# Kernel optimization log

Hardware: AMD Instinct MI355X
Metric: run time of the kernel (lower is better)

Reference implementation:

```python
import jax, jax.numpy as jnp
import numpy as np

N = 50000          # num_nodes
E = 600000         # num_edges
D_IN = 128         # gcn_embed_dims[0]
D_H = 128          # gcn_embed_dims[1]
D_OUT = 64         # gcn_embed_dims[2]
D_MLP = 64         # mlp hidden


def setup_inputs() -> dict:
    key = jax.random.key(0)
    ks = jax.random.split(key, 10)
    s = lambda fan: 1.0 / np.sqrt(fan).astype(np.float32)
    return {
        "X": jax.random.normal(ks[0], (N, D_IN), jnp.float32),
        "edges": jax.random.randint(ks[1], (2, E), 0, N, dtype=jnp.int32),
        # GCN layer 1
        "Wg1": jax.random.normal(ks[2], (D_IN, D_H), jnp.float32) * s(D_IN),
        "bg1": jnp.zeros((D_H,), jnp.float32),
        # GCN layer 2
        "Wg2": jax.random.normal(ks[3], (D_H, D_OUT), jnp.float32) * s(D_H),
        "bg2": jnp.zeros((D_OUT,), jnp.float32),
        # decoder MLP: in = 2*D_OUT = 128
        "Wm1": jax.random.normal(ks[4], (2 * D_OUT, D_MLP), jnp.float32) * s(2 * D_OUT),
        "bm1": jnp.zeros((D_MLP,), jnp.float32),
        "Wm2": jax.random.normal(ks[5], (D_MLP, 1), jnp.float32) * s(D_MLP),
        "bm2": jnp.zeros((1,), jnp.float32),
    }


def gcn_conv(X, W, b, src, dst):
    """GCNConv: out = D^{-1/2} (A + I) D^{-1/2} X W + b (PyG semantics)."""
    n = X.shape[0]
    XW = X @ W                                   # [N, d_out]
    loop = jnp.arange(n, dtype=src.dtype)
    src2 = jnp.concatenate([src, loop])          # add self-loops
    dst2 = jnp.concatenate([dst, loop])
    deg = jax.ops.segment_sum(jnp.ones_like(dst2, dtype=XW.dtype), dst2,
                              num_segments=n)    # in-degree incl. self-loop
    dinv = jax.lax.rsqrt(jnp.maximum(deg, 1.0))  # deg >= 1 due to self-loop
    norm = dinv[src2] * dinv[dst2]               # [E+N]
    out = jax.ops.segment_sum(XW[src2] * norm[:, None], dst2, num_segments=n)
    return out + b


def reference(X, edges, Wg1, bg1, Wg2, bg2, Wm1, bm1, Wm2, bm2):
    src, dst = edges[0], edges[1]
    # encode: GCNConv -> ReLU -> GCNConv
    H = jax.nn.relu(gcn_conv(X, Wg1, bg1, src, dst))
    H = gcn_conv(H, Wg2, bg2, src, dst)          # [N, 64]
    # decode: gather endpoints, concat, MLP
    Z = jnp.concatenate([H[src], H[dst]], axis=-1)  # [E, 128]
    Z = jax.nn.relu(Z @ Wm1 + bm1)                   # [E, 64]
    return Z @ Wm2 + bm2                             # [E, 1]
```

## Files before the change

### kernel.cpp

```cpp
#include <hip/hip_runtime.h>


typedef __attribute__((ext_vector_type(8))) short s8v;
typedef __attribute__((ext_vector_type(4))) float f4v;

__device__ __forceinline__ ushort f2bf(float x) {
    unsigned u = __float_as_uint(x);
    unsigned r = (u + 0x7fffu + ((u >> 16) & 1u)) >> 16;
    return (ushort)r;
}
__device__ __forceinline__ float bf2f(ushort h) {
    return __uint_as_float(((unsigned)h) << 16);
}

__global__ void count_deg_k(const int* __restrict__ dst, int* __restrict__ cnt, int E) {
    int i = blockIdx.x * 256 + threadIdx.x;
    if (i < E) atomicAdd(&cnt[dst[i]], 1);
}

__global__ void dinv_k(const int* __restrict__ cnt, float* __restrict__ dinv, int n) {
    int i = blockIdx.x * 256 + threadIdx.x;
    if (i < n) dinv[i] = rsqrtf((float)cnt[i] + 1.0f);
}

__global__ void scan1_k(const int* __restrict__ cnt, int* __restrict__ excl,
                        int* __restrict__ bsum, int n) {
    __shared__ int sd[256];
    int t = threadIdx.x;
    int base = blockIdx.x * 1024 + t * 4;
    int v0 = 0, v1 = 0, v2 = 0, v3 = 0;
    if (base + 0 < n) v0 = cnt[base + 0];
    if (base + 1 < n) v1 = cnt[base + 1];
    if (base + 2 < n) v2 = cnt[base + 2];
    if (base + 3 < n) v3 = cnt[base + 3];
    int sum = v0 + v1 + v2 + v3;
    int acc = sum;
    sd[t] = acc;
    __syncthreads();
    for (int off = 1; off < 256; off <<= 1) {
        int x = (t >= off) ? sd[t - off] : 0;
        __syncthreads();
        acc += x;
        sd[t] = acc;
        __syncthreads();
    }
    int run = acc - sum;
    if (base + 0 < n) excl[base + 0] = run;
    run += v0;
    if (base + 1 < n) excl[base + 1] = run;
    run += v1;
    if (base + 2 < n) excl[base + 2] = run;
    run += v2;
    if (base + 3 < n) excl[base + 3] = run;
    if (t == 255) bsum[blockIdx.x] = acc;
}

__global__ void scan2_k(int* __restrict__ bsum, int nb) {
    __shared__ int sd[256];
    int t = threadIdx.x;
    int v = (t < nb) ? bsum[t] : 0;
    int acc = v;
    sd[t] = acc;
    __syncthreads();
    for (int off = 1; off < 256; off <<= 1) {
        int x = (t >= off) ? sd[t - off] : 0;
        __syncthreads();
        acc += x;
        sd[t] = acc;
        __syncthreads();
    }
    if (t < nb) bsum[t] = acc - v;
}

__global__ void scan3_k(int* __restrict__ excl, const int* __restrict__ bsum,
                        int* __restrict__ cursor, int n) {
    int i = blockIdx.x * 256 + threadIdx.x;
    if (i < n) {
        int v = excl[i] + bsum[i >> 10];
        excl[i] = v;
        cursor[i] = v;
    }
}

__global__ void scatter_k(const int* __restrict__ src, const int* __restrict__ dst,
                          int* __restrict__ cursor, int2* __restrict__ csr_se, int E) {
    int i = blockIdx.x * 256 + threadIdx.x;
    if (i < E) {
        int d = dst[i];
        int p = atomicAdd(&cursor[d], 1);
        int2 se; se.x = src[i]; se.y = i;
        csr_se[p] = se;
    }
}

__global__ void split_k(const float* __restrict__ X, ushort* __restrict__ Xh,
                        ushort* __restrict__ Xl, int n4) {
    int i = blockIdx.x * 256 + threadIdx.x;
    if (i >= n4) return;
    float4 v = ((const float4*)X)[i];
    ushort4 h, l;
    h.x = f2bf(v.x); l.x = f2bf(v.x - bf2f(h.x));
    h.y = f2bf(v.y); l.y = f2bf(v.y - bf2f(h.y));
    h.z = f2bf(v.z); l.z = f2bf(v.z - bf2f(h.z));
    h.w = f2bf(v.w); l.w = f2bf(v.w - bf2f(h.w));
    ((ushort4*)Xh)[i] = h;
    ((ushort4*)Xl)[i] = l;
}

__global__ void wtsplit_k(const float* __restrict__ W, ushort* __restrict__ Wth,
                          ushort* __restrict__ Wtl) {
    int i = blockIdx.x * 256 + threadIdx.x;
    int n = i >> 7, k = i & 127;
    float x = W[k * 128 + n];
    ushort h = f2bf(x);
    Wth[i] = h;
    Wtl[i] = f2bf(x - bf2f(h));
}

__global__ void wfold_k(const float* __restrict__ Wg2, const float* __restrict__ bg2,
                        const float* __restrict__ Wm1,
                        ushort* __restrict__ Wfth, ushort* __restrict__ Wftl,
                        float* __restrict__ bcat) {
    int i = blockIdx.x * 256 + threadIdx.x;
    if (i < 128 * 128) {
        int r = i >> 7, c = i & 127;
        const float* wc = (c < 64) ? (Wm1 + c) : (Wm1 + 64 * 64 + (c - 64));
        float acc = 0.f;
#pragma unroll 8
        for (int j = 0; j < 64; ++j) acc = fmaf(Wg2[r * 64 + j], wc[j * 64], acc);
        ushort h = f2bf(acc);
        Wfth[c * 128 + r] = h;
        Wftl[c * 128 + r] = f2bf(acc - bf2f(h));
    } else if (i < 128 * 128 + 128) {
        int c = i - 128 * 128;
        const float* wc = (c < 64) ? (Wm1 + c) : (Wm1 + 64 * 64 + (c - 64));
        float acc = 0.f;
#pragma unroll 8
        for (int j = 0; j < 64; ++j) acc = fmaf(bg2[j], wc[j * 64], acc);
        bcat[c] = acc;
    }
}

__global__ __launch_bounds__(256) void mgemm_k(
    const ushort* __restrict__ Ah, const ushort* __restrict__ Al,
    const ushort* __restrict__ Bth, const ushort* __restrict__ Btl,
    const float* __restrict__ rowscale, float* __restrict__ C, int M) {
    __shared__ ushort Bs[2][128][136];
    const int t = threadIdx.x;
#pragma unroll
    for (int i = 0; i < 16; ++i) {
        int c = i * 256 + t;
        int arr = c >> 11;
        int cc = c & 2047;
        int n = cc >> 4, kb = cc & 15;
        const ushort* src = arr ? Btl : Bth;
        s8v v = *(const s8v*)(src + n * 128 + kb * 8);
        *(s8v*)(&Bs[arr][n][kb * 8]) = v;
    }
    __syncthreads();

    const int lane = t & 63;
    const int w = t >> 6;
    const int r16 = lane & 15;
    const int kg = lane >> 4;
    int arow = blockIdx.x * 64 + w * 16 + r16;
    if (arow >= M) arow = M - 1;
    const ushort* pAh = Ah + (size_t)arow * 128 + kg * 8;
    const ushort* pAl = Al + (size_t)arow * 128 + kg * 8;

    f4v acc[8];
#pragma unroll
    for (int ct = 0; ct < 8; ++ct) acc[ct] = (f4v){0.f, 0.f, 0.f, 0.f};

#pragma unroll
    for (int ks = 0; ks < 4; ++ks) {
        s8v ah = *(const s8v*)(pAh + ks * 32);
        s8v al = *(const s8v*)(pAl + ks * 32);
#pragma unroll
        for (int ct = 0; ct < 8; ++ct) {
            s8v bh = *(const s8v*)(&Bs[0][ct * 16 + r16][ks * 32 + kg * 8]);
            s8v bl = *(const s8v*)(&Bs[1][ct * 16 + r16][ks * 32 + kg * 8]);
            acc[ct] = __builtin_amdgcn_mfma_f32_16x16x32_bf16(ah, bh, acc[ct], 0, 0, 0);
            acc[ct] = __builtin_amdgcn_mfma_f32_16x16x32_bf16(ah, bl, acc[ct], 0, 0, 0);
            acc[ct] = __builtin_amdgcn_mfma_f32_16x16x32_bf16(al, bh, acc[ct], 0, 0, 0);
        }
    }

    const int rbase = blockIdx.x * 64 + w * 16 + kg * 4;
#pragma unroll
    for (int r = 0; r < 4; ++r) {
        int row = rbase + r;
        if (row < M) {
            float sc = rowscale[row];
#pragma unroll
            for (int ct = 0; ct < 8; ++ct)
                C[(size_t)row * 128 + ct * 16 + r16] = acc[ct][r] * sc;
        }
    }
}

template <bool RELU_BF16>
__global__ void agg128_k(const float* __restrict__ XW, const float* __restrict__ dinv,
                         const int* __restrict__ row_start, const int* __restrict__ cnt,
                         const int2* __restrict__ csr_se, const float* __restrict__ bias,
                         float* __restrict__ outf, ushort* __restrict__ outh,
                         ushort* __restrict__ outl, int n) {
    int wid = (int)((blockIdx.x * blockDim.x + threadIdx.x) >> 6);
    int lane = threadIdx.x & 63;
    if (wid >= n) return;
    float di = dinv[wid];
    int deg = cnt[wid];
    int rs = row_start[wid];
    const float2* base = (const float2*)XW;
    float2 a = base[(size_t)wid * 64 + lane];
    float ax = a.x, ay = a.y;
    int i = 0;
    while (i < deg) {
        int take = deg - i;
        if (take > 64) take = 64;
        int addr = rs + i + lane;
        int lim = rs + deg - 1;
        if (addr > lim) addr = lim;
        int vidx = csr_se[addr].x;
        int j = 0;
        for (; j + 8 <= take; j += 8) {
            int s0 = __shfl(vidx, j + 0), s1 = __shfl(vidx, j + 1);
            int s2 = __shfl(vidx, j + 2), s3 = __shfl(vidx, j + 3);
            int s4 = __shfl(vidx, j + 4), s5 = __shfl(vidx, j + 5);
            int s6 = __shfl(vidx, j + 6), s7 = __shfl(vidx, j + 7);
            float2 u0 = base[(size_t)s0 * 64 + lane];
            float2 u1 = base[(size_t)s1 * 64 + lane];
            float2 u2 = base[(size_t)s2 * 64 + lane];
            float2 u3 = base[(size_t)s3 * 64 + lane];
            float2 u4 = base[(size_t)s4 * 64 + lane];
            float2 u5 = base[(size_t)s5 * 64 + lane];
            float2 u6 = base[(size_t)s6 * 64 + lane];
            float2 u7 = base[(size_t)s7 * 64 + lane];
            ax += ((u0.x + u1.x) + (u2.x + u3.x)) + ((u4.x + u5.x) + (u6.x + u7.x));
            ay += ((u0.y + u1.y) + (u2.y + u3.y)) + ((u4.y + u5.y) + (u6.y + u7.y));
        }
        for (; j + 2 <= take; j += 2) {
            int s0 = __shfl(vidx, j + 0), s1 = __shfl(vidx, j + 1);
            float2 u0 = base[(size_t)s0 * 64 + lane];
            float2 u1 = base[(size_t)s1 * 64 + lane];
            ax += u0.x + u1.x;
            ay += u0.y + u1.y;
        }
        if (j < take) {
            int s = __shfl(vidx, j);
            float2 u = base[(size_t)s * 64 + lane];
            ax += u.x;
            ay += u.y;
        }
        i += take;
    }
    float2 b = ((const float2*)bias)[lane];
    ax = fmaf(ax, di, b.x);
    ay = fmaf(ay, di, b.y);
    if constexpr (RELU_BF16) {
        ax = fmaxf(ax, 0.f);
        ay = fmaxf(ay, 0.f);
        ushort2 h, l;
        h.x = f2bf(ax); l.x = f2bf(ax - bf2f(h.x));
        h.y = f2bf(ay); l.y = f2bf(ay - bf2f(h.y));
        ((ushort2*)outh)[(size_t)wid * 64 + lane] = h;
        ((ushort2*)outl)[(size_t)wid * 64 + lane] = l;
    } else {
        float2 r; r.x = ax; r.y = ay;
        ((float2*)outf)[(size_t)wid * 64 + lane] = r;
    }
}

__global__ __launch_bounds__(256) void edge_mlp2_k(
    const float* __restrict__ PQ, const int* __restrict__ row_start,
    const int* __restrict__ cnt, const int2* __restrict__ csr_se,
    const float* __restrict__ bm1, const float* __restrict__ w2,
    const float* __restrict__ bm2, float* __restrict__ out, int n) {
    int wid = (int)((blockIdx.x * blockDim.x + threadIdx.x) >> 6);
    int lane = threadIdx.x & 63;
    if (wid >= n) return;
    int deg = cnt[wid];
    if (deg == 0) return;
    int rs = row_start[wid];
    const int sub = lane >> 4;
    const int q = lane & 15;

    const float4 b1v = ((const float4*)bm1)[q];
    const float4 w2v = ((const float4*)w2)[q];
    const float b2 = bm2[0];
    float4 Qv = *(const float4*)(PQ + (size_t)wid * 128 + 64 + q * 4);
    float4 bq;
    bq.x = Qv.x + b1v.x; bq.y = Qv.y + b1v.y;
    bq.z = Qv.z + b1v.z; bq.w = Qv.w + b1v.w;

    int i = 0;
    while (i < deg) {
        int take = deg - i;
        if (take > 64) take = 64;
        int addr = rs + i + lane;
        int lim = rs + deg - 1;
        if (addr > lim) addr = lim;
        int2 se = csr_se[addr];
        for (int j = 0; j < take; j += 8) {
            int ia = j + sub;
            int ib = j + 4 + sub;
            bool aa = ia < take;
            bool ab = ib < take;
            int sa = __shfl(se.x, aa ? ia : 0);
            int ea = __shfl(se.y, aa ? ia : 0);
            int sb = __shfl(se.x, ab ? ib : 0);
            int eb = __shfl(se.y, ab ? ib : 0);
            float4 pa = *(const float4*)(PQ + (size_t)sa * 128 + q * 4);
            float4 pb = *(const float4*)(PQ + (size_t)sb * 128 + q * 4);
            float ha0 = fmaxf(pa.x + bq.x, 0.f);
            float ha1 = fmaxf(pa.y + bq.y, 0.f);
            float ha2 = fmaxf(pa.z + bq.z, 0.f);
            float ha3 = fmaxf(pa.w + bq.w, 0.f);
            float hb0 = fmaxf(pb.x + bq.x, 0.f);
            float hb1 = fmaxf(pb.y + bq.y, 0.f);
            float hb2 = fmaxf(pb.z + bq.z, 0.f);
            float hb3 = fmaxf(pb.w + bq.w, 0.f);
            float va = fmaf(ha0, w2v.x, fmaf(ha1, w2v.y, fmaf(ha2, w2v.z, ha3 * w2v.w)));
            float vb = fmaf(hb0, w2v.x, fmaf(hb1, w2v.y, fmaf(hb2, w2v.z, hb3 * w2v.w)));
            va += __shfl_xor(va, 8, 16);
            va += __shfl_xor(va, 4, 16);
            va += __shfl_xor(va, 2, 16);
            va += __shfl_xor(va, 1, 16);
            vb += __shfl_xor(vb, 8, 16);
            vb += __shfl_xor(vb, 4, 16);
            vb += __shfl_xor(vb, 2, 16);
            vb += __shfl_xor(vb, 1, 16);
            if (aa && q == 0) out[ea] = va + b2;
            if (ab && q == 0) out[eb] = vb + b2;
        }
        i += take;
    }
}


extern "C" void kernel_launch(void* const* d_in, const int* in_sizes, int n_in,
                              void* d_out, int out_size, void* d_ws, size_t ws_size,
                              hipStream_t stream) {
    const float* X   = (const float*)d_in[0];
    const int*  edges = (const int*)d_in[1];
    const float* Wg1 = (const float*)d_in[2];
    const float* bg1 = (const float*)d_in[3];
    const float* Wg2 = (const float*)d_in[4];
    const float* bg2 = (const float*)d_in[5];
    const float* Wm1 = (const float*)d_in[6];
    const float* bm1 = (const float*)d_in[7];
    const float* Wm2 = (const float*)d_in[8];
    const float* bm2 = (const float*)d_in[9];
    float* out = (float*)d_out;

    const int N = in_sizes[0] / 128;
    const int E = in_sizes[1] / 2;
    const int* esrc = edges;
    const int* edst = edges + E;

    char* p = (char*)d_ws;
    auto alloc = [&](size_t nbytes) {
        void* r = (void*)p;
        p += (nbytes + 255) & ~(size_t)255;
        return r;
    };
    float* bufA   = (float*)alloc((size_t)N * 128 * 4);
    float* bufB   = (float*)alloc((size_t)N * 128 * 4);
    float* dinv   = (float*)alloc((size_t)N * 4);
    int* cnt      = (int*)alloc((size_t)N * 4);
    int* rowst    = (int*)alloc((size_t)N * 4);
    int* cursor   = (int*)alloc((size_t)N * 4);
    int* bsum     = (int*)alloc(1024);
    ushort* Wg1th = (ushort*)alloc(128 * 128 * 2);
    ushort* Wg1tl = (ushort*)alloc(128 * 128 * 2);
    ushort* Wfth  = (ushort*)alloc(128 * 128 * 2);
    ushort* Wftl  = (ushort*)alloc(128 * 128 * 2);
    float* bcat   = (float*)alloc(128 * 4);
    int2* csr_se  = (int2*)alloc((size_t)E * 8);
    (void)ws_size; (void)n_in; (void)out_size;

    const size_t NF = (size_t)N * 128;
    ushort* Xh = (ushort*)bufB;
    ushort* Xl = Xh + NF;
    ushort* Hh = Xh;
    ushort* Hl = Xl;

    const int gE = (E + 255) / 256;
    const int gN = (N + 255) / 256;
    const int nb = (N + 1023) / 1024;
    const int gM64 = (N + 63) / 64;
    const int gAgg = (N * 64 + 255) / 256;
    const int n4 = (int)(NF / 4);
    const int gSplit = (n4 + 255) / 256;

    hipMemsetAsync(cnt, 0, (size_t)N * 4, stream);
    count_deg_k<<<gE, 256, 0, stream>>>(edst, cnt, E);
    dinv_k<<<gN, 256, 0, stream>>>(cnt, dinv, N);
    scan1_k<<<nb, 256, 0, stream>>>(cnt, rowst, bsum, N);
    scan2_k<<<1, 256, 0, stream>>>(bsum, nb);
    scan3_k<<<gN, 256, 0, stream>>>(rowst, bsum, cursor, N);
    scatter_k<<<gE, 256, 0, stream>>>(esrc, edst, cursor, csr_se, E);
    wtsplit_k<<<64, 256, 0, stream>>>(Wg1, Wg1th, Wg1tl);
    wfold_k<<<65, 256, 0, stream>>>(Wg2, bg2, Wm1, Wfth, Wftl, bcat);
    split_k<<<gSplit, 256, 0, stream>>>(X, Xh, Xl, n4);

    mgemm_k<<<gM64, 256, 0, stream>>>(Xh, Xl, Wg1th, Wg1tl, dinv, bufA, N);
    agg128_k<true><<<gAgg, 256, 0, stream>>>(bufA, dinv, rowst, cnt, csr_se, bg1,
                                             nullptr, Hh, Hl, N);
    mgemm_k<<<gM64, 256, 0, stream>>>(Hh, Hl, Wfth, Wftl, dinv, bufA, N);
    agg128_k<false><<<gAgg, 256, 0, stream>>>(bufA, dinv, rowst, cnt, csr_se, bcat,
                                              bufB, nullptr, nullptr, N);
    edge_mlp2_k<<<gAgg, 256, 0, stream>>>(bufB, rowst, cnt, csr_se, bm1, Wm2, bm2, out, N);
}
```

Baseline: 314.0 us.

## Fuse bf16 split into GEMM and store intermediate features as bf16

```diff
diff --git a/kernel.cpp b/kernel.cpp
--- a/kernel.cpp
+++ b/kernel.cpp
@@ -1,30 +1,30 @@
 #include <hip/hip_runtime.h>
 
 
-typedef __attribute__((ext_vector_type(8))) short s8v;
-typedef __attribute__((ext_vector_type(4))) float f4v;
-
-__device__ __forceinline__ ushort f2bf(float x) {
+typedef __attribute__((ext_vector_type(8))) short bf8v;
+typedef __attribute__((ext_vector_type(4))) float fa4v;
+
+__device__ __forceinline__ ushort to_bf(float x) {
     unsigned u = __float_as_uint(x);
     unsigned r = (u + 0x7fffu + ((u >> 16) & 1u)) >> 16;
     return (ushort)r;
 }
-__device__ __forceinline__ float bf2f(ushort h) {
+__device__ __forceinline__ float from_bf(ushort h) {
     return __uint_as_float(((unsigned)h) << 16);
 }
 
-__global__ void count_deg_k(const int* __restrict__ dst, int* __restrict__ cnt, int E) {
+__global__ void deg_count_k(const int* __restrict__ dst, int* __restrict__ cnt, int E) {
     int i = blockIdx.x * 256 + threadIdx.x;
     if (i < E) atomicAdd(&cnt[dst[i]], 1);
 }
 
-__global__ void dinv_k(const int* __restrict__ cnt, float* __restrict__ dinv, int n) {
+__global__ void deg_inv_k(const int* __restrict__ cnt, float* __restrict__ dinv, int n) {
     int i = blockIdx.x * 256 + threadIdx.x;
     if (i < n) dinv[i] = rsqrtf((float)cnt[i] + 1.0f);
 }
 
-__global__ void scan1_k(const int* __restrict__ cnt, int* __restrict__ excl,
-                        int* __restrict__ bsum, int n) {
+__global__ void scan_a_k(const int* __restrict__ cnt, int* __restrict__ excl,
+                         int* __restrict__ bsum, int n) {
     __shared__ int sd[256];
     int t = threadIdx.x;
     int base = blockIdx.x * 1024 + t * 4;
@@ -55,7 +55,7 @@
     if (t == 255) bsum[blockIdx.x] = acc;
 }
 
-__global__ void scan2_k(int* __restrict__ bsum, int nb) {
+__global__ void scan_b_k(int* __restrict__ bsum, int nb) {
     __shared__ int sd[256];
     int t = threadIdx.x;
     int v = (t < nb) ? bsum[t] : 0;
@@ -72,8 +72,8 @@
     if (t < nb) bsum[t] = acc - v;
 }
 
-__global__ void scan3_k(int* __restrict__ excl, const int* __restrict__ bsum,
-                        int* __restrict__ cursor, int n) {
+__global__ void scan_c_k(int* __restrict__ excl, const int* __restrict__ bsum,
+                         int* __restrict__ cursor, int n) {
     int i = blockIdx.x * 256 + threadIdx.x;
     if (i < n) {
         int v = excl[i] + bsum[i >> 10];
@@ -82,8 +82,8 @@
     }
 }
 
-__global__ void scatter_k(const int* __restrict__ src, const int* __restrict__ dst,
-                          int* __restrict__ cursor, int2* __restrict__ csr_se, int E) {
+__global__ void csr_fill_k(const int* __restrict__ src, const int* __restrict__ dst,
+                           int* __restrict__ cursor, int2* __restrict__ csr_se, int E) {
     int i = blockIdx.x * 256 + threadIdx.x;
     if (i < E) {
         int d = dst[i];
@@ -93,34 +93,20 @@
     }
 }
 
-__global__ void split_k(const float* __restrict__ X, ushort* __restrict__ Xh,
-                        ushort* __restrict__ Xl, int n4) {
-    int i = blockIdx.x * 256 + threadIdx.x;
-    if (i >= n4) return;
-    float4 v = ((const float4*)X)[i];
-    ushort4 h, l;
-    h.x = f2bf(v.x); l.x = f2bf(v.x - bf2f(h.x));
-    h.y = f2bf(v.y); l.y = f2bf(v.y - bf2f(h.y));
-    h.z = f2bf(v.z); l.z = f2bf(v.z - bf2f(h.z));
-    h.w = f2bf(v.w); l.w = f2bf(v.w - bf2f(h.w));
-    ((ushort4*)Xh)[i] = h;
-    ((ushort4*)Xl)[i] = l;
-}
-
-__global__ void wtsplit_k(const float* __restrict__ W, ushort* __restrict__ Wth,
-                          ushort* __restrict__ Wtl) {
+__global__ void w1t_split_k(const float* __restrict__ W, ushort* __restrict__ Wth,
+                            ushort* __restrict__ Wtl) {
     int i = blockIdx.x * 256 + threadIdx.x;
     int n = i >> 7, k = i & 127;
     float x = W[k * 128 + n];
-    ushort h = f2bf(x);
+    ushort h = to_bf(x);
     Wth[i] = h;
-    Wtl[i] = f2bf(x - bf2f(h));
-}
-
-__global__ void wfold_k(const float* __restrict__ Wg2, const float* __restrict__ bg2,
-                        const float* __restrict__ Wm1,
-                        ushort* __restrict__ Wfth, ushort* __restrict__ Wftl,
-                        float* __restrict__ bcat) {
+    Wtl[i] = to_bf(x - from_bf(h));
+}
+
+__global__ void wfold_split_k(const float* __restrict__ Wg2, const float* __restrict__ bg2,
+                              const float* __restrict__ Wm1,
+                              ushort* __restrict__ Wfth, ushort* __restrict__ Wftl,
+                              float* __restrict__ bcat) {
     int i = blockIdx.x * 256 + threadIdx.x;
     if (i < 128 * 128) {
         int r = i >> 7, c = i & 127;
@@ -128,9 +114,9 @@
         float acc = 0.f;
 #pragma unroll 8
         for (int j = 0; j < 64; ++j) acc = fmaf(Wg2[r * 64 + j], wc[j * 64], acc);
-        ushort h = f2bf(acc);
+        ushort h = to_bf(acc);
         Wfth[c * 128 + r] = h;
-        Wftl[c * 128 + r] = f2bf(acc - bf2f(h));
+        Wftl[c * 128 + r] = to_bf(acc - from_bf(h));
     } else if (i < 128 * 128 + 128) {
         int c = i - 128 * 128;
         const float* wc = (c < 64) ? (Wm1 + c) : (Wm1 + 64 * 64 + (c - 64));
@@ -141,10 +127,10 @@
     }
 }
 
-__global__ __launch_bounds__(256) void mgemm_k(
-    const ushort* __restrict__ Ah, const ushort* __restrict__ Al,
+__global__ __launch_bounds__(256) void gemm_mfma_k(
+    const float* __restrict__ A,
     const ushort* __restrict__ Bth, const ushort* __restrict__ Btl,
-    const float* __restrict__ rowscale, float* __restrict__ C, int M) {
+    const float* __restrict__ rowscale, ushort* __restrict__ C, int M) {
     __shared__ ushort Bs[2][128][136];
     const int t = threadIdx.x;
 #pragma unroll
@@ -154,8 +140,8 @@
         int cc = c & 2047;
         int n = cc >> 4, kb = cc & 15;
         const ushort* src = arr ? Btl : Bth;
-        s8v v = *(const s8v*)(src + n * 128 + kb * 8);
-        *(s8v*)(&Bs[arr][n][kb * 8]) = v;
+        bf8v v = *(const bf8v*)(src + n * 128 + kb * 8);
+        *(bf8v*)(&Bs[arr][n][kb * 8]) = v;
     }
     __syncthreads();
 
@@ -165,21 +151,28 @@
     const int kg = lane >> 4;
     int arow = blockIdx.x * 64 + w * 16 + r16;
     if (arow >= M) arow = M - 1;
-    const ushort* pAh = Ah + (size_t)arow * 128 + kg * 8;
-    const ushort* pAl = Al + (size_t)arow * 128 + kg * 8;
-
-    f4v acc[8];
-#pragma unroll
-    for (int ct = 0; ct < 8; ++ct) acc[ct] = (f4v){0.f, 0.f, 0.f, 0.f};
+    const float* pA = A + (size_t)arow * 128 + kg * 8;
+
+    fa4v acc[8];
+#pragma unroll
+    for (int ct = 0; ct < 8; ++ct) acc[ct] = (fa4v){0.f, 0.f, 0.f, 0.f};
 
 #pragma unroll
     for (int ks = 0; ks < 4; ++ks) {
-        s8v ah = *(const s8v*)(pAh + ks * 32);
-        s8v al = *(const s8v*)(pAl + ks * 32);
+        float av[8];
+        *(float4*)(&av[0]) = *(const float4*)(pA + ks * 32);
+        *(float4*)(&av[4]) = *(const float4*)(pA + ks * 32 + 4);
+        bf8v ah, al;
+#pragma unroll
+        for (int j = 0; j < 8; ++j) {
+            ushort h = to_bf(av[j]);
+            ah[j] = (short)h;
+            al[j] = (short)to_bf(av[j] - from_bf(h));
+        }
 #pragma unroll
         for (int ct = 0; ct < 8; ++ct) {
-            s8v bh = *(const s8v*)(&Bs[0][ct * 16 + r16][ks * 32 + kg * 8]);
-            s8v bl = *(const s8v*)(&Bs[1][ct * 16 + r16][ks * 32 + kg * 8]);
+            bf8v bh = *(const bf8v*)(&Bs[0][ct * 16 + r16][ks * 32 + kg * 8]);
+            bf8v bl = *(const bf8v*)(&Bs[1][ct * 16 + r16][ks * 32 + kg * 8]);
             acc[ct] = __builtin_amdgcn_mfma_f32_16x16x32_bf16(ah, bh, acc[ct], 0, 0, 0);
             acc[ct] = __builtin_amdgcn_mfma_f32_16x16x32_bf16(ah, bl, acc[ct], 0, 0, 0);
             acc[ct] = __builtin_amdgcn_mfma_f32_16x16x32_bf16(al, bh, acc[ct], 0, 0, 0);
@@ -194,26 +187,24 @@
             float sc = rowscale[row];
 #pragma unroll
             for (int ct = 0; ct < 8; ++ct)
-                C[(size_t)row * 128 + ct * 16 + r16] = acc[ct][r] * sc;
-        }
-    }
-}
-
-template <bool RELU_BF16>
-__global__ void agg128_k(const float* __restrict__ XW, const float* __restrict__ dinv,
-                         const int* __restrict__ row_start, const int* __restrict__ cnt,
-                         const int2* __restrict__ csr_se, const float* __restrict__ bias,
-                         float* __restrict__ outf, ushort* __restrict__ outh,
-                         ushort* __restrict__ outl, int n) {
+                C[(size_t)row * 128 + ct * 16 + r16] = to_bf(acc[ct][r] * sc);
+        }
+    }
+}
+
+template <bool RELU, bool BF16OUT>
+__global__ void gcn_agg_k(const ushort* __restrict__ Cb, const float* __restrict__ dinv,
+                          const int* __restrict__ row_start, const int* __restrict__ cnt,
+                          const int2* __restrict__ csr_se, const float* __restrict__ bias,
+                          float* __restrict__ outf, ushort* __restrict__ outh, int n) {
     int wid = (int)((blockIdx.x * blockDim.x + threadIdx.x) >> 6);
     int lane = threadIdx.x & 63;
     if (wid >= n) return;
     float di = dinv[wid];
     int deg = cnt[wid];
     int rs = row_start[wid];
-    const float2* base = (const float2*)XW;
-    float2 a = base[(size_t)wid * 64 + lane];
-    float ax = a.x, ay = a.y;
+    ushort2 a = *(const ushort2*)(Cb + (size_t)wid * 128 + lane * 2);
+    float ax = from_bf(a.x), ay = from_bf(a.y);
     int i = 0;
     while (i < deg) {
         int take = deg - i;
@@ -228,51 +219,54 @@
             int s2 = __shfl(vidx, j + 2), s3 = __shfl(vidx, j + 3);
             int s4 = __shfl(vidx, j + 4), s5 = __shfl(vidx, j + 5);
             int s6 = __shfl(vidx, j + 6), s7 = __shfl(vidx, j + 7);
-            float2 u0 = base[(size_t)s0 * 64 + lane];
-            float2 u1 = base[(size_t)s1 * 64 + lane];
-            float2 u2 = base[(size_t)s2 * 64 + lane];
-            float2 u3 = base[(size_t)s3 * 64 + lane];
-            float2 u4 = base[(size_t)s4 * 64 + lane];
-            float2 u5 = base[(size_t)s5 * 64 + lane];
-            float2 u6 = base[(size_t)s6 * 64 + lane];
-            float2 u7 = base[(size_t)s7 * 64 + lane];
-            ax += ((u0.x + u1.x) + (u2.x + u3.x)) + ((u4.x + u5.x) + (u6.x + u7.x));
-            ay += ((u0.y + u1.y) + (u2.y + u3.y)) + ((u4.y + u5.y) + (u6.y + u7.y));
+            ushort2 u0 = *(const ushort2*)(Cb + (size_t)s0 * 128 + lane * 2);
+            ushort2 u1 = *(const ushort2*)(Cb + (size_t)s1 * 128 + lane * 2);
+            ushort2 u2 = *(const ushort2*)(Cb + (size_t)s2 * 128 + lane * 2);
+            ushort2 u3 = *(const ushort2*)(Cb + (size_t)s3 * 128 + lane * 2);
+            ushort2 u4 = *(const ushort2*)(Cb + (size_t)s4 * 128 + lane * 2);
+            ushort2 u5 = *(const ushort2*)(Cb + (size_t)s5 * 128 + lane * 2);
+            ushort2 u6 = *(const ushort2*)(Cb + (size_t)s6 * 128 + lane * 2);
+            ushort2 u7 = *(const ushort2*)(Cb + (size_t)s7 * 128 + lane * 2);
+            ax += ((from_bf(u0.x) + from_bf(u1.x)) + (from_bf(u2.x) + from_bf(u3.x))) +
+                  ((from_bf(u4.x) + from_bf(u5.x)) + (from_bf(u6.x) + from_bf(u7.x)));
+            ay += ((from_bf(u0.y) + from_bf(u1.y)) + (from_bf(u2.y) + from_bf(u3.y))) +
+                  ((from_bf(u4.y) + from_bf(u5.y)) + (from_bf(u6.y) + from_bf(u7.y)));
         }
         for (; j + 2 <= take; j += 2) {
             int s0 = __shfl(vidx, j + 0), s1 = __shfl(vidx, j + 1);
-            float2 u0 = base[(size_t)s0 * 64 + lane];
-            float2 u1 = base[(size_t)s1 * 64 + lane];
-            ax += u0.x + u1.x;
-            ay += u0.y + u1.y;
+            ushort2 u0 = *(const ushort2*)(Cb + (size_t)s0 * 128 + lane * 2);
+            ushort2 u1 = *(const ushort2*)(Cb + (size_t)s1 * 128 + lane * 2);
+            ax += from_bf(u0.x) + from_bf(u1.x);
+            ay += from_bf(u0.y) + from_bf(u1.y);
         }
         if (j < take) {
             int s = __shfl(vidx, j);
-            float2 u = base[(size_t)s * 64 + lane];
-            ax += u.x;
-            ay += u.y;
+            ushort2 u = *(const ushort2*)(Cb + (size_t)s * 128 + lane * 2);
+            ax += from_bf(u.x);
+            ay += from_bf(u.y);
         }
         i += take;
     }
     float2 b = ((const float2*)bias)[lane];
     ax = fmaf(ax, di, b.x);
     ay = fmaf(ay, di, b.y);
-    if constexpr (RELU_BF16) {
+    if constexpr (RELU) {
         ax = fmaxf(ax, 0.f);
         ay = fmaxf(ay, 0.f);
-        ushort2 h, l;
-        h.x = f2bf(ax); l.x = f2bf(ax - bf2f(h.x));
-        h.y = f2bf(ay); l.y = f2bf(ay - bf2f(h.y));
+    }
+    if constexpr (BF16OUT) {
+        ushort2 h;
+        h.x = to_bf(ax);
+        h.y = to_bf(ay);
         ((ushort2*)outh)[(size_t)wid * 64 + lane] = h;
-        ((ushort2*)outl)[(size_t)wid * 64 + lane] = l;
     } else {
         float2 r; r.x = ax; r.y = ay;
         ((float2*)outf)[(size_t)wid * 64 + lane] = r;
     }
 }
 
-__global__ __launch_bounds__(256) void edge_mlp2_k(
-    const float* __restrict__ PQ, const int* __restrict__ row_start,
+__global__ __launch_bounds__(256) void edge_dec_k(
+    const ushort* __restrict__ PQ, const int* __restrict__ row_start,
     const int* __restrict__ cnt, const int2* __restrict__ csr_se,
     const float* __restrict__ bm1, const float* __restrict__ w2,
     const float* __restrict__ bm2, float* __restrict__ out, int n) {
@@ -288,10 +282,10 @@
     const float4 b1v = ((const float4*)bm1)[q];
     const float4 w2v = ((const float4*)w2)[q];
     const float b2 = bm2[0];
-    float4 Qv = *(const float4*)(PQ + (size_t)wid * 128 + 64 + q * 4);
+    ushort4 Qu = *(const ushort4*)(PQ + (size_t)wid * 128 + 64 + q * 4);
     float4 bq;
-    bq.x = Qv.x + b1v.x; bq.y = Qv.y + b1v.y;
-    bq.z = Qv.z + b1v.z; bq.w = Qv.w + b1v.w;
+    bq.x = from_bf(Qu.x) + b1v.x; bq.y = from_bf(Qu.y) + b1v.y;
+    bq.z = from_bf(Qu.z) + b1v.z; bq.w = from_bf(Qu.w) + b1v.w;
 
     int i = 0;
     while (i < deg) {
@@ -310,16 +304,16 @@
             int ea = __shfl(se.y, aa ? ia : 0);
             int sb = __shfl(se.x, ab ? ib : 0);
             int eb = __shfl(se.y, ab ? ib : 0);
-            float4 pa = *(const float4*)(PQ + (size_t)sa * 128 + q * 4);
-            float4 pb = *(const float4*)(PQ + (size_t)sb * 128 + q * 4);
-            float ha0 = fmaxf(pa.x + bq.x, 0.f);
-            float ha1 = fmaxf(pa.y + bq.y, 0.f);
-            float ha2 = fmaxf(pa.z + bq.z, 0.f);
-            float ha3 = fmaxf(pa.w + bq.w, 0.f);
-            float hb0 = fmaxf(pb.x + bq.x, 0.f);
-            float hb1 = fmaxf(pb.y + bq.y, 0.f);
-            float hb2 = fmaxf(pb.z + bq.z, 0.f);
-            float hb3 = fmaxf(pb.w + bq.w, 0.f);
+            ushort4 pua = *(const ushort4*)(PQ + (size_t)sa * 128 + q * 4);
+            ushort4 pub = *(const ushort4*)(PQ + (size_t)sb * 128 + q * 4);
+            float ha0 = fmaxf(from_bf(pua.x) + bq.x, 0.f);
+            float ha1 = fmaxf(from_bf(pua.y) + bq.y, 0.f);
+            float ha2 = fmaxf(from_bf(pua.z) + bq.z, 0.f);
+            float ha3 = fmaxf(from_bf(pua.w) + bq.w, 0.f);
+            float hb0 = fmaxf(from_bf(pub.x) + bq.x, 0.f);
+            float hb1 = fmaxf(from_bf(pub.y) + bq.y, 0.f);
+            float hb2 = fmaxf(from_bf(pub.z) + bq.z, 0.f);
+            float hb3 = fmaxf(from_bf(pub.w) + bq.w, 0.f);
             float va = fmaf(ha0, w2v.x, fmaf(ha1, w2v.y, fmaf(ha2, w2v.z, ha3 * w2v.w)));
             float vb = fmaf(hb0, w2v.x, fmaf(hb1, w2v.y, fmaf(hb2, w2v.z, hb3 * w2v.w)));
             va += __shfl_xor(va, 8, 16);
@@ -364,8 +358,9 @@
         p += (nbytes + 255) & ~(size_t)255;
         return r;
     };
-    float* bufA   = (float*)alloc((size_t)N * 128 * 4);
-    float* bufB   = (float*)alloc((size_t)N * 128 * 4);
+    float* H      = (float*)alloc((size_t)N * 128 * 4);
+    ushort* Cb    = (ushort*)alloc((size_t)N * 128 * 2);
+    ushort* PQ    = (ushort*)alloc((size_t)N * 128 * 2);
     float* dinv   = (float*)alloc((size_t)N * 4);
     int* cnt      = (int*)alloc((size_t)N * 4);
     int* rowst    = (int*)alloc((size_t)N * 4);
@@ -379,36 +374,27 @@
     int2* csr_se  = (int2*)alloc((size_t)E * 8);
     (void)ws_size; (void)n_in; (void)out_size;
 
-    const size_t NF = (size_t)N * 128;
-    ushort* Xh = (ushort*)bufB;
-    ushort* Xl = Xh + NF;
-    ushort* Hh = Xh;
-    ushort* Hl = Xl;
-
     const int gE = (E + 255) / 256;
     const int gN = (N + 255) / 256;
     const int nb = (N + 1023) / 1024;
     const int gM64 = (N + 63) / 64;
     const int gAgg = (N * 64 + 255) / 256;
-    const int n4 = (int)(NF / 4);
-    const int gSplit = (n4 + 255) / 256;
 
     hipMemsetAsync(cnt, 0, (size_t)N * 4, stream);
-    count_deg_k<<<gE, 256, 0, stream>>>(edst, cnt, E);
-    dinv_k<<<gN, 256, 0, stream>>>(cnt, dinv, N);
-    scan1_k<<<nb, 256, 0, stream>>>(cnt, rowst, bsum, N);
-    scan2_k<<<1, 256, 0, stream>>>(bsum, nb);
-    scan3_k<<<gN, 256, 0, stream>>>(rowst, bsum, cursor, N);
-    scatter_k<<<gE, 256, 0, stream>>>(esrc, edst, cursor, csr_se, E);
-    wtsplit_k<<<64, 256, 0, stream>>>(Wg1, Wg1th, Wg1tl);
-    wfold_k<<<65, 256, 0, stream>>>(Wg2, bg2, Wm1, Wfth, Wftl, bcat);
-    split_k<<<gSplit, 256, 0, stream>>>(X, Xh, Xl, n4);
-
-    mgemm_k<<<gM64, 256, 0, stream>>>(Xh, Xl, Wg1th, Wg1tl, dinv, bufA, N);
-    agg128_k<true><<<gAgg, 256, 0, stream>>>(bufA, dinv, rowst, cnt, csr_se, bg1,
-                                             nullptr, Hh, Hl, N);
-    mgemm_k<<<gM64, 256, 0, stream>>>(Hh, Hl, Wfth, Wftl, dinv, bufA, N);
-    agg128_k<false><<<gAgg, 256, 0, stream>>>(bufA, dinv, rowst, cnt, csr_se, bcat,
-                                              bufB, nullptr, nullptr, N);
-    edge_mlp2_k<<<gAgg, 256, 0, stream>>>(bufB, rowst, cnt, csr_se, bm1, Wm2, bm2, out, N);
-}
+    deg_count_k<<<gE, 256, 0, stream>>>(edst, cnt, E);
+    deg_inv_k<<<gN, 256, 0, stream>>>(cnt, dinv, N);
+    scan_a_k<<<nb, 256, 0, stream>>>(cnt, rowst, bsum, N);
+    scan_b_k<<<1, 256, 0, stream>>>(bsum, nb);
+    scan_c_k<<<gN, 256, 0, stream>>>(rowst, bsum, cursor, N);
+    csr_fill_k<<<gE, 256, 0, stream>>>(esrc, edst, cursor, csr_se, E);
+    w1t_split_k<<<64, 256, 0, stream>>>(Wg1, Wg1th, Wg1tl);
+    wfold_split_k<<<65, 256, 0, stream>>>(Wg2, bg2, Wm1, Wfth, Wftl, bcat);
+
+    gemm_mfma_k<<<gM64, 256, 0, stream>>>(X, Wg1th, Wg1tl, dinv, Cb, N);
+    gcn_agg_k<true, false><<<gAgg, 256, 0, stream>>>(Cb, dinv, rowst, cnt, csr_se, bg1,
+                                                     H, nullptr, N);
+    gemm_mfma_k<<<gM64, 256, 0, stream>>>(H, Wfth, Wftl, dinv, Cb, N);
+    gcn_agg_k<false, true><<<gAgg, 256, 0, stream>>>(Cb, dinv, rowst, cnt, csr_se, bcat,
+                                                     nullptr, PQ, N);
+    edge_dec_k<<<gAgg, 256, 0, stream>>>(PQ, rowst, cnt, csr_se, bm1, Wm2, bm2, out, N);
+}
```

Measured after the change: 272.4 us. 1.15x faster.
